# Kernel optimization log

Hardware: AMD Instinct MI355X
Metric: run time of the kernel (lower is better)

The kernel has to match this reference:

```python
import jax, jax.numpy as jnp
import numpy as np

EPS = 1e-8
NUM_HEADS = 8
SCALE = 25.0
SIM_THRESH = 0.75
BLOCK = 10  # per-frame proposal group size used by the zeroing mask


def _l2norm(x):
    return x / (jnp.linalg.norm(x, axis=-1, keepdims=True) + EPS)


def setup_inputs() -> dict:
    key = jax.random.key(0)
    ks = jax.random.split(key, 7)
    B, N, C = 1, 2000, 256
    H = NUM_HEADS
    x_cls = jax.random.normal(ks[0], (B, N, C), dtype=jnp.float32)
    x_reg = jax.random.normal(ks[1], (B, N, C), dtype=jnp.float32)
    cls_score = jax.random.uniform(ks[2], (N,), dtype=jnp.float32)
    fg_score = jax.random.uniform(ks[3], (N,), dtype=jnp.float32)
    coord_attn = jax.random.uniform(ks[4], (B, H, N, N), dtype=jnp.float32)
    W_qkv_cls = jax.random.normal(ks[5], (3 * C, C), dtype=jnp.float32) * 0.02
    W_qkv_reg = jax.random.normal(ks[6], (3 * C, C), dtype=jnp.float32) * 0.02
    return {"x_cls": x_cls, "x_reg": x_reg, "cls_score": cls_score,
            "fg_score": fg_score, "coord_attn": coord_attn,
            "W_qkv_cls": W_qkv_cls, "W_qkv_reg": W_qkv_reg}


def reference(x_cls, x_reg, cls_score, fg_score, coord_attn, W_qkv_cls, W_qkv_reg):
    B, N, C = x_cls.shape
    H = NUM_HEADS
    D = C // H

    def qkv(x, W):
        t = (x @ W.T).reshape(B, N, 3, H, D).transpose(2, 0, 3, 1, 4)  # [3,B,H,N,D]
        return t[0], t[1], t[2]

    q_cls, k_cls, v_cls = qkv(x_cls, W_qkv_cls)
    q_reg, k_reg, v_reg = qkv(x_reg, W_qkv_reg)

    q_cls, k_cls = _l2norm(q_cls), _l2norm(k_cls)
    q_reg, k_reg = _l2norm(q_reg), _l2norm(k_reg)
    v_cls_normed = _l2norm(v_cls)

    cs = cls_score.reshape(1, 1, 1, N)  # broadcast over [B,H,N,N]
    fs = fg_score.reshape(1, 1, 1, N)

    attn_cls_raw = jnp.einsum('bhnd,bhmd->bhnm', v_cls_normed, v_cls_normed)

    attn_cls = jax.nn.softmax(jnp.einsum('bhnd,bhmd->bhnm', q_cls, k_cls) * SCALE * cs, axis=-1)
    attn_reg = jax.nn.softmax(jnp.einsum('bhnd,bhmd->bhnm', q_reg, k_reg) * SCALE * fs, axis=-1)

    attn = (attn_reg + attn_cls) * 0.5 * coord_attn
    attn = jax.lax.stop_gradient(attn)  # original detaches before masking

    # block-diagonal zeroing: row j zeros cols [j//10*10, j//10*10+9), keep diagonal
    rows = jnp.arange(N)[:, None]
    cols = jnp.arange(N)[None, :]
    block_start = (rows // BLOCK) * BLOCK
    zero_mask = (cols >= block_start) & (cols < block_start + (BLOCK - 1)) & (cols != rows)
    attn = jnp.where(zero_mask, 0.0, attn)

    x = jnp.einsum('bhnm,bhmd->bhnd', attn, v_cls).transpose(0, 2, 1, 3).reshape(B, N, C)
    x_ori = v_cls.transpose(0, 2, 1, 3).reshape(B, N, C)
    x_cat = jnp.concatenate([x, x_ori], axis=-1)  # [B,N,2C]

    # ave=True branch
    sim_raw = jnp.sum(attn_cls_raw, axis=1)[0] / H          # [N,N]
    sim_mask = (sim_raw > SIM_THRESH).astype(x_cls.dtype)
    sim_attn = jnp.sum(attn, axis=1)[0] / H                 # [N,N]
    sim_round2 = jax.nn.softmax(sim_attn, axis=-1)
    sim_round2 = sim_mask * sim_round2 / (jnp.sum(sim_mask * sim_round2, axis=-1, keepdims=True) + EPS)
    return x_cat, sim_round2
```

## Files before the change

kernel.cpp:

```cpp
#include <hip/hip_runtime.h>
#include <math.h>

typedef _Float16 half8 __attribute__((ext_vector_type(8)));
typedef _Float16 half4 __attribute__((ext_vector_type(4)));
typedef float f32x4 __attribute__((ext_vector_type(4)));

constexpr int N = 2000;
constexpr int NP = 2048;
constexpr int H = 8;
constexpr int D = 32;
constexpr float SCL = 25.0f;
constexpr float FM = 25.0f;

#define MFMA16(a,b,c) __builtin_amdgcn_mfma_f32_16x16x32_f16((a),(b),(c),0,0,0)


__global__ __launch_bounds__(256) void wconv_kernel(
    const float* __restrict__ Wc, const float* __restrict__ Wr,
    _Float16* __restrict__ Wch, _Float16* __restrict__ Wrh)
{
    const int i = blockIdx.x * 256 + threadIdx.x;
    Wch[i] = (_Float16)Wc[i];
    Wrh[i] = (_Float16)Wr[i];
}

__global__ __launch_bounds__(256) void qkv_kernel(
    const float* __restrict__ xc, const float* __restrict__ xr,
    const _Float16* __restrict__ Wch, const _Float16* __restrict__ Wrh,
    _Float16* __restrict__ Qch, _Float16* __restrict__ Kch,
    _Float16* __restrict__ Qrh, _Float16* __restrict__ Krh,
    _Float16* __restrict__ Vnh, _Float16* __restrict__ Vth,
    float* __restrict__ out)
{
    constexpr int XS = 264;
    __shared__ _Float16 xs[16 * XS];
    const int t = threadIdx.x;
    const int n0 = blockIdx.x * 16;
    const int by = blockIdx.y;
    const int which = (by < 3) ? by : (by - 3);
    const bool isCls = by < 3;
    const float* x = isCls ? xc : xr;
    const _Float16* Wh = isCls ? Wch : Wrh;

    #pragma unroll
    for (int it = 0; it < 4; ++it) {
        const int f = t + it * 256;
        const int row = f >> 6, c4 = f & 63;
        const float4 v = *(const float4*)(x + (size_t)(n0 + row) * 256 + c4 * 4);
        half4 hv; hv[0]=(_Float16)v.x; hv[1]=(_Float16)v.y; hv[2]=(_Float16)v.z; hv[3]=(_Float16)v.w;
        *(half4*)&xs[row * XS + c4 * 4] = hv;
    }
    __syncthreads();

    const int w = t >> 6, l = t & 63;
    const int lr = l & 15, lg = l >> 4;
    const int obase = which * 256 + w * 64;
    f32x4 acc[4] = {{0,0,0,0},{0,0,0,0},{0,0,0,0},{0,0,0,0}};
    for (int k0 = 0; k0 < 256; k0 += 32) {
        const half8 aX = *(const half8*)&xs[lr * XS + k0 + lg * 8];
        #pragma unroll
        for (int s = 0; s < 4; ++s) {
            const half8 bW = *(const half8*)(Wh + (size_t)(obase + s * 16 + lr) * 256 + k0 + lg * 8);
            acc[s] = MFMA16(aX, bW, acc[s]);
        }
    }
    #pragma unroll
    for (int p = 0; p < 2; ++p) {
        const int h = 2 * w + p;
        float ss[4];
        #pragma unroll
        for (int j = 0; j < 4; ++j) {
            float v = acc[2*p][j]*acc[2*p][j] + acc[2*p+1][j]*acc[2*p+1][j];
            #pragma unroll
            for (int off = 1; off < 16; off <<= 1) v += __shfl_xor(v, off);
            ss[j] = sqrtf(v) + 1e-8f;
        }
        if (which < 2) {
            _Float16* Qd = isCls ? (which == 0 ? Qch : Kch) : (which == 0 ? Qrh : Krh);
            #pragma unroll
            for (int sh = 0; sh < 2; ++sh)
                #pragma unroll
                for (int j = 0; j < 4; ++j)
                    Qd[((size_t)h*NP + n0 + lg*4 + j)*D + sh*16 + lr] = (_Float16)(acc[2*p+sh][j] / ss[j]);
        } else {
            #pragma unroll
            for (int sh = 0; sh < 2; ++sh) {
                const int d = sh * 16 + lr;
                half4 tv;
                #pragma unroll
                for (int j = 0; j < 4; ++j) {
                    const float raw = acc[2*p+sh][j];
                    Vnh[((size_t)h*NP + n0 + lg*4 + j)*D + d] = (_Float16)(raw / ss[j]);
                    out[(size_t)(n0 + lg*4 + j)*512 + 256 + h*D + d] = raw;
                    tv[j] = (_Float16)raw;
                }
                *(half4*)(Vth + ((size_t)h*D + d)*NP + n0 + lg*4) = tv;
            }
        }
    }
}

__global__ __launch_bounds__(512) void stats_kernel(
    const _Float16* __restrict__ Qch, const _Float16* __restrict__ Kch,
    const _Float16* __restrict__ Qrh, const _Float16* __restrict__ Krh,
    const float* __restrict__ clsScore, const float* __restrict__ fgScore,
    float* __restrict__ ST)
{
    __shared__ float Ssh[4][2][16];
    const int t = threadIdx.x;
    const int w = t >> 6, l = t & 63;
    const int nsub = w >> 1, mhalf = w & 1;
    const int n0 = blockIdx.x * 64 + nsub * 16;
    const int h = blockIdx.y, z = blockIdx.z;
    const _Float16* Q = z ? Qrh : Qch;
    const _Float16* K = z ? Krh : Kch;
    const float* score = z ? fgScore : clsScore;
    const int lr = l & 15, lg = l >> 4;
    const half8 aQ = *(const half8*)(Q + ((size_t)h*NP + n0 + lr)*D + lg*8);
    float S[4] = {0.f, 0.f, 0.f, 0.f};
    const int msBeg = mhalf ? 63 : 0;
    const int msEnd = mhalf ? 125 : 63;
    for (int ms = msBeg; ms < msEnd; ++ms) {
        const int m = ms * 16 + lr;
        const half8 bK = *(const half8*)(K + ((size_t)h*NP + m)*D + lg*8);
        f32x4 z4 = {0.f, 0.f, 0.f, 0.f};
        const f32x4 c = MFMA16(aQ, bK, z4);
        const float sm = SCL * score[m];
        #pragma unroll
        for (int j = 0; j < 4; ++j) S[j] += __expf(fmaf(c[j], sm, -FM));
    }
    #pragma unroll
    for (int j = 0; j < 4; ++j) {
        #pragma unroll
        for (int off = 1; off < 16; off <<= 1) S[j] += __shfl_xor(S[j], off);
    }
    if (lr == 0) {
        #pragma unroll
        for (int j = 0; j < 4; ++j) Ssh[nsub][mhalf][lg*4 + j] = S[j];
    }
    __syncthreads();
    if (t < 64) {
        const int ns = t >> 4, rl = t & 15;
        ST[((size_t)z*H + h)*NP + blockIdx.x*64 + ns*16 + rl] = Ssh[ns][0][rl] + Ssh[ns][1][rl];
    }
}

__global__ __launch_bounds__(256) void vvmask_kernel(
    const _Float16* __restrict__ Vnh, unsigned char* __restrict__ Mask)
{
    const int t = threadIdx.x;
    const int w = t >> 6, l = t & 63;
    const int n0 = blockIdx.y * 16;
    const int m00 = blockIdx.x * 256 + w * 64;
    const int lr = l & 15, lg = l >> 4;
    half8 aV[8];
    #pragma unroll
    for (int h = 0; h < 8; ++h)
        aV[h] = *(const half8*)(Vnh + ((size_t)(h*NP + n0 + lr))*D + lg*8);
    for (int s = 0; s < 4; ++s) {
        const int mb = m00 + s*16;
        f32x4 acc = {0.f, 0.f, 0.f, 0.f};
        #pragma unroll
        for (int h = 0; h < 8; ++h) {
            const half8 bV = *(const half8*)(Vnh + ((size_t)(h*NP + mb + lr))*D + lg*8);
            acc = MFMA16(aV[h], bV, acc);
        }
        const int m = mb + lr;
        if (m < N) {
            #pragma unroll
            for (int j = 0; j < 4; ++j) {
                const int n = n0 + lg*4 + j;
                Mask[(size_t)n*N + m] = (acc[j]*0.125f > 0.75f) ? (unsigned char)1 : (unsigned char)0;
            }
        }
    }
}

__global__ __launch_bounds__(256) void attn_kernel(
    const _Float16* __restrict__ Qch, const _Float16* __restrict__ Kch,
    const _Float16* __restrict__ Qrh, const _Float16* __restrict__ Krh,
    const _Float16* __restrict__ Vth, const float* __restrict__ coord,
    const float* __restrict__ clsScore, const float* __restrict__ fgScore,
    const float* __restrict__ ST,
    float* __restrict__ SIM, _Float16* __restrict__ XPH)
{
    constexpr int AP = 136;
    __shared__ _Float16 att_s[16 * AP];
    __shared__ _Float16 pvred[4][2][16][18];
    __shared__ float st_s[2][H][16];

    const int t = threadIdx.x;
    const int w = t >> 6, l = t & 63;
    const int mc = blockIdx.x;
    const int m0 = mc * 128;
    const int n0 = blockIdx.y * 16;
    const int lr = l & 15, lg = l >> 4;
    const int colbase = w * 32;

    {
        const int z = t >> 7, h = (t >> 4) & 7, r = t & 15;
        st_s[z][h][r] = 1.f / ST[((size_t)z*H + h)*NP + n0 + r];
    }
    int mI[2]; bool mOk[2]; float sC[2], sF[2];
    #pragma unroll
    for (int s = 0; s < 2; ++s) {
        mI[s] = m0 + colbase + s*16 + lr;
        mOk[s] = mI[s] < N;
        sC[s] = mOk[s] ? SCL * clsScore[mI[s]] : 0.f;
        sF[s] = mOk[s] ? SCL * fgScore[mI[s]] : 0.f;
    }
    int nj[4], bsj[4];
    #pragma unroll
    for (int j = 0; j < 4; ++j) { nj[j] = n0 + lg*4 + j; bsj[j] = (nj[j]/10)*10; }
    float simacc[2][4] = {{0,0,0,0},{0,0,0,0}};
    __syncthreads();

    for (int h = 0; h < H; ++h) {
        float co[2][4];
        #pragma unroll
        for (int s = 0; s < 2; ++s)
            #pragma unroll
            for (int j = 0; j < 4; ++j)
                co[s][j] = mOk[s] ? coord[((size_t)h*N + nj[j])*N + mI[s]] : 0.f;

        const half8 aQc = *(const half8*)(Qch + ((size_t)h*NP + n0 + lr)*D + lg*8);
        const half8 aQr = *(const half8*)(Qrh + ((size_t)h*NP + n0 + lr)*D + lg*8);
        float iC[4], iR[4];
        #pragma unroll
        for (int j = 0; j < 4; ++j) { iC[j] = st_s[0][h][lg*4+j]; iR[j] = st_s[1][h][lg*4+j]; }

        #pragma unroll
        for (int s = 0; s < 2; ++s) {
            const int mb = m0 + colbase + s*16;
            const half8 bKc = *(const half8*)(Kch + ((size_t)h*NP + mb + lr)*D + lg*8);
            const half8 bKr = *(const half8*)(Krh + ((size_t)h*NP + mb + lr)*D + lg*8);
            f32x4 z4 = {0.f, 0.f, 0.f, 0.f};
            const f32x4 cc = MFMA16(aQc, bKc, z4);
            const f32x4 cr = MFMA16(aQr, bKr, z4);
            #pragma unroll
            for (int j = 0; j < 4; ++j) {
                float a = 0.f;
                if (mOk[s]) {
                    const float eC = __expf(fmaf(cc[j], sC[s], -FM)) * iC[j];
                    const float eR = __expf(fmaf(cr[j], sF[s], -FM)) * iR[j];
                    a = (eC + eR) * 0.5f * co[s][j];
                    if (mI[s] >= bsj[j] && mI[s] < bsj[j]+9 && mI[s] != nj[j]) a = 0.f;
                }
                att_s[(lg*4+j)*AP + colbase + s*16 + lr] = (_Float16)a;
                simacc[s][j] += a;
            }
        }
        f32x4 pv0 = {0.f,0.f,0.f,0.f}, pv1 = {0.f,0.f,0.f,0.f};
        {
            const half8 aA  = *(const half8*)&att_s[lr*AP + colbase + lg*8];
            const half8 bV0 = *(const half8*)(Vth + ((size_t)h*D + lr)*NP + m0 + colbase + lg*8);
            const half8 bV1 = *(const half8*)(Vth + ((size_t)h*D + 16 + lr)*NP + m0 + colbase + lg*8);
            pv0 = MFMA16(aA, bV0, pv0);
            pv1 = MFMA16(aA, bV1, pv1);
        }
        #pragma unroll
        for (int j = 0; j < 4; ++j) {
            pvred[w][0][lg*4+j][lr] = (_Float16)pv0[j];
            pvred[w][1][lg*4+j][lr] = (_Float16)pv1[j];
        }
        __syncthreads();
        #pragma unroll
        for (int e = t; e < 512; e += 256) {
            const int db = e >> 8, r = (e >> 4) & 15, d0 = e & 15;
            const float sum = (float)pvred[0][db][r][d0] + (float)pvred[1][db][r][d0]
                            + (float)pvred[2][db][r][d0] + (float)pvred[3][db][r][d0];
            XPH[(((size_t)mc*H + h)*N + n0 + r)*D + db*16 + d0] = (_Float16)sum;
        }
        __syncthreads();
    }
    #pragma unroll
    for (int s = 0; s < 2; ++s) {
        if (!mOk[s]) continue;
        #pragma unroll
        for (int j = 0; j < 4; ++j)
            SIM[(size_t)nj[j]*N + mI[s]] = simacc[s][j] * 0.125f;
    }
}

__global__ __launch_bounds__(256) void reduce_kernel(
    const _Float16* __restrict__ XPH, float* __restrict__ out)
{
    const int n = blockIdx.x, t = threadIdx.x;
    const int h = t >> 5, d = t & 31;
    float acc = 0.f;
    #pragma unroll
    for (int mcI = 0; mcI < 16; ++mcI)
        acc += (float)XPH[(((size_t)mcI*H + h)*N + n)*D + d];
    out[(size_t)n*512 + t] = acc;
}

__global__ __launch_bounds__(256) void simfinal_kernel(
    const float* __restrict__ SIM, const unsigned char* __restrict__ Mask,
    float* __restrict__ out)
{
    __shared__ float4 buf[500];
    __shared__ float redA[4], redB[4];
    const int n = blockIdx.x, t = threadIdx.x;
    const float4* row4 = (const float4*)(SIM + (size_t)n*N);
    const uchar4* mrow4 = (const uchar4*)(Mask + (size_t)n*N);
    float mx = -1e30f;
    for (int i = t; i < 500; i += 256) {
        const float4 v = row4[i];
        buf[i] = v;
        mx = fmaxf(mx, fmaxf(fmaxf(v.x, v.y), fmaxf(v.z, v.w)));
    }
    #pragma unroll
    for (int off = 1; off < 64; off <<= 1) mx = fmaxf(mx, __shfl_xor(mx, off));
    const int wv = t >> 6;
    if ((t & 63) == 0) redA[wv] = mx;
    __syncthreads();
    const float M = fmaxf(fmaxf(redA[0], redA[1]), fmaxf(redA[2], redA[3]));
    float sA = 0.f, sM = 0.f;
    for (int i = t; i < 500; i += 256) {
        float4 v = buf[i];
        const uchar4 mk = mrow4[i];
        v.x = __expf(v.x - M); v.y = __expf(v.y - M);
        v.z = __expf(v.z - M); v.w = __expf(v.w - M);
        buf[i] = v;
        sA += v.x + v.y + v.z + v.w;
        sM += (mk.x ? v.x : 0.f) + (mk.y ? v.y : 0.f) + (mk.z ? v.z : 0.f) + (mk.w ? v.w : 0.f);
    }
    #pragma unroll
    for (int off = 1; off < 64; off <<= 1) { sA += __shfl_xor(sA, off); sM += __shfl_xor(sM, off); }
    __syncthreads();
    if ((t & 63) == 0) { redA[wv] = sA; redB[wv] = sM; }
    __syncthreads();
    const float SA = redA[0] + redA[1] + redA[2] + redA[3];
    const float SMK = redB[0] + redB[1] + redB[2] + redB[3];
    const float inv = 1.f / (SMK + 1e-8f * SA);
    float4* orow = (float4*)(out + 1024000 + (size_t)n*N);
    for (int i = t; i < 500; i += 256) {
        const float4 v = buf[i];
        const uchar4 mk = mrow4[i];
        orow[i] = make_float4(mk.x ? v.x * inv : 0.f, mk.y ? v.y * inv : 0.f,
                              mk.z ? v.z * inv : 0.f, mk.w ? v.w * inv : 0.f);
    }
}

extern "C" void kernel_launch(void* const* d_in, const int* in_sizes, int n_in,
                              void* d_out, int out_size, void* d_ws, size_t ws_size,
                              hipStream_t stream) {
    const float* x_cls     = (const float*)d_in[0];
    const float* x_reg     = (const float*)d_in[1];
    const float* cls_score = (const float*)d_in[2];
    const float* fg_score  = (const float*)d_in[3];
    const float* coord     = (const float*)d_in[4];
    const float* Wc        = (const float*)d_in[5];
    const float* Wr        = (const float*)d_in[6];

    char* base = (char*)d_ws;
    float* ST       = (float*)base;
    float* SIM      = (float*)(base + 131072);
    _Float16* XPH   = (_Float16*)(base + 16131072);
    _Float16* Qch   = (_Float16*)(base + 32515072);
    _Float16* Kch   = Qch + 524288;
    _Float16* Qrh   = Qch + 2*524288;
    _Float16* Krh   = Qch + 3*524288;
    _Float16* Vnh   = Qch + 4*524288;
    _Float16* Vth   = Qch + 5*524288;
    _Float16* Wch   = (_Float16*)(base + 38806528);
    _Float16* Wrh   = (_Float16*)(base + 39199744);
    unsigned char* Mask = (unsigned char*)(base + 39592960);
    float* out = (float*)d_out;

    hipMemsetAsync(Qch, 0, 6*1048576, stream);
    wconv_kernel<<<768, 256, 0, stream>>>(Wc, Wr, Wch, Wrh);
    qkv_kernel<<<dim3(125, 5), 256, 0, stream>>>(x_cls, x_reg, Wch, Wrh,
                                                 Qch, Kch, Qrh, Krh, Vnh, Vth, out);
    stats_kernel<<<dim3(32, 8, 2), 512, 0, stream>>>(Qch, Kch, Qrh, Krh, cls_score, fg_score, ST);
    vvmask_kernel<<<dim3(8, 125), 256, 0, stream>>>(Vnh, Mask);
    attn_kernel<<<dim3(16, 125), 256, 0, stream>>>(Qch, Kch, Qrh, Krh, Vth, coord,
                                                   cls_score, fg_score, ST, SIM, XPH);
    reduce_kernel<<<2000, 256, 0, stream>>>(XPH, out);
    simfinal_kernel<<<2000, 256, 0, stream>>>(SIM, Mask, out);
}
```

Measured before the change: 137.6 us.

## Transpose attention MFMA layout to keep scores in registers and remove LDS round-trip

The QK MFMA operands are swapped so each lane holds four consecutive key columns for one query row. The attention fragment then feeds the PV MFMA (16x16x16) directly from registers, with no LDS staging of att_s. This also allows vectorized coalesced coord, score and SIM accesses, plus prefetching of the next head's coord tile. Per-head barriers are dropped by keeping all head partials in a larger LDS buffer and reducing once at the end. Each block now covers 256 columns, halving the XPH partials, and the stats kernel stores reciprocals. The trade-offs are more registers and more LDS per block.

```diff
diff --git a/kernel.cpp b/kernel.cpp
--- a/kernel.cpp
+++ b/kernel.cpp
@@ -12,7 +12,8 @@
 constexpr float SCL = 25.0f;
 constexpr float FM = 25.0f;
 
-#define MFMA16(a,b,c) __builtin_amdgcn_mfma_f32_16x16x32_f16((a),(b),(c),0,0,0)
+#define MFMA16(a,b,c)  __builtin_amdgcn_mfma_f32_16x16x32_f16((a),(b),(c),0,0,0)
+#define MFMA16K(a,b,c) __builtin_amdgcn_mfma_f32_16x16x16f16((a),(b),(c),0,0,0)
 
 
 __global__ __launch_bounds__(256) void wconv_kernel(
@@ -104,7 +105,7 @@
     const _Float16* __restrict__ Qch, const _Float16* __restrict__ Kch,
     const _Float16* __restrict__ Qrh, const _Float16* __restrict__ Krh,
     const float* __restrict__ clsScore, const float* __restrict__ fgScore,
-    float* __restrict__ ST)
+    float* __restrict__ STi)
 {
     __shared__ float Ssh[4][2][16];
     const int t = threadIdx.x;
@@ -141,7 +142,8 @@
     __syncthreads();
     if (t < 64) {
         const int ns = t >> 4, rl = t & 15;
-        ST[((size_t)z*H + h)*NP + blockIdx.x*64 + ns*16 + rl] = Ssh[ns][0][rl] + Ssh[ns][1][rl];
+        STi[((size_t)z*H + h)*NP + blockIdx.x*64 + ns*16 + rl]
+            = 1.f / (Ssh[ns][0][rl] + Ssh[ns][1][rl]);
     }
 }
 
@@ -181,104 +183,101 @@
     const _Float16* __restrict__ Qrh, const _Float16* __restrict__ Krh,
     const _Float16* __restrict__ Vth, const float* __restrict__ coord,
     const float* __restrict__ clsScore, const float* __restrict__ fgScore,
-    const float* __restrict__ ST,
+    const float* __restrict__ STi,
     float* __restrict__ SIM, _Float16* __restrict__ XPH)
 {
-    constexpr int AP = 136;
-    __shared__ _Float16 att_s[16 * AP];
-    __shared__ _Float16 pvred[4][2][16][18];
-    __shared__ float st_s[2][H][16];
+    __shared__ _Float16 pvred[4][H][2][16][17];
 
     const int t = threadIdx.x;
     const int w = t >> 6, l = t & 63;
+    const int lr = l & 15, lg = l >> 4;
     const int mc = blockIdx.x;
-    const int m0 = mc * 128;
+    const int m0 = mc * 256;
     const int n0 = blockIdx.y * 16;
-    const int lr = l & 15, lg = l >> 4;
-    const int colbase = w * 32;
-
-    {
-        const int z = t >> 7, h = (t >> 4) & 7, r = t & 15;
-        st_s[z][h][r] = 1.f / ST[((size_t)z*H + h)*NP + n0 + r];
-    }
-    int mI[2]; bool mOk[2]; float sC[2], sF[2];
-    #pragma unroll
-    for (int s = 0; s < 2; ++s) {
-        mI[s] = m0 + colbase + s*16 + lr;
-        mOk[s] = mI[s] < N;
-        sC[s] = mOk[s] ? SCL * clsScore[mI[s]] : 0.f;
-        sF[s] = mOk[s] ? SCL * fgScore[mI[s]] : 0.f;
-    }
-    int nj[4], bsj[4];
-    #pragma unroll
-    for (int j = 0; j < 4; ++j) { nj[j] = n0 + lg*4 + j; bsj[j] = (nj[j]/10)*10; }
-    float simacc[2][4] = {{0,0,0,0},{0,0,0,0}};
-    __syncthreads();
+    const int n  = n0 + lr;
+    const int bs = (n / 10) * 10;
+    const int cb = w * 64;
+
+    int mb[4]; bool ok[4];
+    #pragma unroll
+    for (int s = 0; s < 4; ++s) { mb[s] = m0 + cb + s*16; ok[s] = mb[s] < N; }
+
+    float simacc[4][4];
+    #pragma unroll
+    for (int s = 0; s < 4; ++s)
+        #pragma unroll
+        for (int j = 0; j < 4; ++j) simacc[s][j] = 0.f;
+
+    f32x4 co[4];
+    #pragma unroll
+    for (int s = 0; s < 4; ++s)
+        co[s] = ok[s] ? *(const f32x4*)(coord + (size_t)n*N + mb[s] + lg*4)
+                      : (f32x4){0.f,0.f,0.f,0.f};
 
     for (int h = 0; h < H; ++h) {
-        float co[2][4];
-        #pragma unroll
-        for (int s = 0; s < 2; ++s)
-            #pragma unroll
-            for (int j = 0; j < 4; ++j)
-                co[s][j] = mOk[s] ? coord[((size_t)h*N + nj[j])*N + mI[s]] : 0.f;
-
-        const half8 aQc = *(const half8*)(Qch + ((size_t)h*NP + n0 + lr)*D + lg*8);
-        const half8 aQr = *(const half8*)(Qrh + ((size_t)h*NP + n0 + lr)*D + lg*8);
-        float iC[4], iR[4];
-        #pragma unroll
-        for (int j = 0; j < 4; ++j) { iC[j] = st_s[0][h][lg*4+j]; iR[j] = st_s[1][h][lg*4+j]; }
-
-        #pragma unroll
-        for (int s = 0; s < 2; ++s) {
-            const int mb = m0 + colbase + s*16;
-            const half8 bKc = *(const half8*)(Kch + ((size_t)h*NP + mb + lr)*D + lg*8);
-            const half8 bKr = *(const half8*)(Krh + ((size_t)h*NP + mb + lr)*D + lg*8);
-            f32x4 z4 = {0.f, 0.f, 0.f, 0.f};
-            const f32x4 cc = MFMA16(aQc, bKc, z4);
-            const f32x4 cr = MFMA16(aQr, bKr, z4);
+        f32x4 coN[4];
+        if (h < H-1) {
+            #pragma unroll
+            for (int s = 0; s < 4; ++s)
+                coN[s] = ok[s] ? *(const f32x4*)(coord + ((size_t)(h+1)*N + n)*N + mb[s] + lg*4)
+                               : (f32x4){0.f,0.f,0.f,0.f};
+        }
+        const float iC = STi[((size_t)0*H + h)*NP + n];
+        const float iR = STi[((size_t)1*H + h)*NP + n];
+        const half8 aQc = *(const half8*)(Qch + ((size_t)h*NP + n)*D + lg*8);
+        const half8 aQr = *(const half8*)(Qrh + ((size_t)h*NP + n)*D + lg*8);
+
+        f32x4 pv0 = {0.f,0.f,0.f,0.f}, pv1 = {0.f,0.f,0.f,0.f};
+        #pragma unroll
+        for (int s = 0; s < 4; ++s) {
+            if (!ok[s]) continue;
+            const half8 bKc = *(const half8*)(Kch + ((size_t)h*NP + mb[s] + lr)*D + lg*8);
+            const half8 bKr = *(const half8*)(Krh + ((size_t)h*NP + mb[s] + lr)*D + lg*8);
+            f32x4 z4 = {0.f,0.f,0.f,0.f};
+            const f32x4 cc = MFMA16(bKc, aQc, z4);
+            const f32x4 cr = MFMA16(bKr, aQr, z4);
+            const f32x4 sc4 = *(const f32x4*)(clsScore + mb[s] + lg*4);
+            const f32x4 sf4 = *(const f32x4*)(fgScore + mb[s] + lg*4);
+            half4 af;
             #pragma unroll
             for (int j = 0; j < 4; ++j) {
-                float a = 0.f;
-                if (mOk[s]) {
-                    const float eC = __expf(fmaf(cc[j], sC[s], -FM)) * iC[j];
-                    const float eR = __expf(fmaf(cr[j], sF[s], -FM)) * iR[j];
-                    a = (eC + eR) * 0.5f * co[s][j];
-                    if (mI[s] >= bsj[j] && mI[s] < bsj[j]+9 && mI[s] != nj[j]) a = 0.f;
-                }
-                att_s[(lg*4+j)*AP + colbase + s*16 + lr] = (_Float16)a;
+                const int m = mb[s] + lg*4 + j;
+                float a = (__expf(fmaf(cc[j], SCL*sc4[j], -FM)) * iC
+                         + __expf(fmaf(cr[j], SCL*sf4[j], -FM)) * iR) * 0.5f * co[s][j];
+                if (m >= bs && m < bs+9 && m != n) a = 0.f;
                 simacc[s][j] += a;
+                af[j] = (_Float16)a;
             }
-        }
-        f32x4 pv0 = {0.f,0.f,0.f,0.f}, pv1 = {0.f,0.f,0.f,0.f};
-        {
-            const half8 aA  = *(const half8*)&att_s[lr*AP + colbase + lg*8];
-            const half8 bV0 = *(const half8*)(Vth + ((size_t)h*D + lr)*NP + m0 + colbase + lg*8);
-            const half8 bV1 = *(const half8*)(Vth + ((size_t)h*D + 16 + lr)*NP + m0 + colbase + lg*8);
-            pv0 = MFMA16(aA, bV0, pv0);
-            pv1 = MFMA16(aA, bV1, pv1);
+            const half4 bV0 = *(const half4*)(Vth + ((size_t)h*D + lr)*NP + mb[s] + lg*4);
+            const half4 bV1 = *(const half4*)(Vth + ((size_t)h*D + 16 + lr)*NP + mb[s] + lg*4);
+            pv0 = MFMA16K(af, bV0, pv0);
+            pv1 = MFMA16K(af, bV1, pv1);
         }
         #pragma unroll
         for (int j = 0; j < 4; ++j) {
-            pvred[w][0][lg*4+j][lr] = (_Float16)pv0[j];
-            pvred[w][1][lg*4+j][lr] = (_Float16)pv1[j];
-        }
-        __syncthreads();
-        #pragma unroll
-        for (int e = t; e < 512; e += 256) {
-            const int db = e >> 8, r = (e >> 4) & 15, d0 = e & 15;
-            const float sum = (float)pvred[0][db][r][d0] + (float)pvred[1][db][r][d0]
-                            + (float)pvred[2][db][r][d0] + (float)pvred[3][db][r][d0];
-            XPH[(((size_t)mc*H + h)*N + n0 + r)*D + db*16 + d0] = (_Float16)sum;
-        }
-        __syncthreads();
-    }
-    #pragma unroll
-    for (int s = 0; s < 2; ++s) {
-        if (!mOk[s]) continue;
-        #pragma unroll
-        for (int j = 0; j < 4; ++j)
-            SIM[(size_t)nj[j]*N + mI[s]] = simacc[s][j] * 0.125f;
+            pvred[w][h][0][lg*4 + j][lr] = (_Float16)pv0[j];
+            pvred[w][h][1][lg*4 + j][lr] = (_Float16)pv1[j];
+        }
+        #pragma unroll
+        for (int s = 0; s < 4; ++s) co[s] = coN[s];
+    }
+
+    __syncthreads();
+
+    for (int e = t; e < 4096; e += 256) {
+        const int hh = e >> 9, db = (e >> 8) & 1, r = (e >> 4) & 15, d0 = e & 15;
+        const float sum = (float)pvred[0][hh][db][r][d0] + (float)pvred[1][hh][db][r][d0]
+                        + (float)pvred[2][hh][db][r][d0] + (float)pvred[3][hh][db][r][d0];
+        XPH[(((size_t)mc*H + hh)*N + n0 + r)*D + db*16 + d0] = (_Float16)sum;
+    }
+
+    #pragma unroll
+    for (int s = 0; s < 4; ++s) {
+        if (!ok[s]) continue;
+        f32x4 v;
+        #pragma unroll
+        for (int j = 0; j < 4; ++j) v[j] = simacc[s][j] * 0.125f;
+        *(f32x4*)(SIM + (size_t)n*N + mb[s] + lg*4) = v;
     }
 }
 
@@ -289,7 +288,7 @@
     const int h = t >> 5, d = t & 31;
     float acc = 0.f;
     #pragma unroll
-    for (int mcI = 0; mcI < 16; ++mcI)
+    for (int mcI = 0; mcI < 8; ++mcI)
         acc += (float)XPH[(((size_t)mcI*H + h)*N + n)*D + d];
     out[(size_t)n*512 + t] = acc;
 }
@@ -354,28 +353,28 @@
     const float* Wr        = (const float*)d_in[6];
 
     char* base = (char*)d_ws;
-    float* ST       = (float*)base;
+    float* STi      = (float*)base;
     float* SIM      = (float*)(base + 131072);
     _Float16* XPH   = (_Float16*)(base + 16131072);
-    _Float16* Qch   = (_Float16*)(base + 32515072);
+    _Float16* Qch   = (_Float16*)(base + 24323072);
     _Float16* Kch   = Qch + 524288;
     _Float16* Qrh   = Qch + 2*524288;
     _Float16* Krh   = Qch + 3*524288;
     _Float16* Vnh   = Qch + 4*524288;
     _Float16* Vth   = Qch + 5*524288;
-    _Float16* Wch   = (_Float16*)(base + 38806528);
-    _Float16* Wrh   = (_Float16*)(base + 39199744);
-    unsigned char* Mask = (unsigned char*)(base + 39592960);
+    _Float16* Wch   = (_Float16*)(base + 30614528);
+    _Float16* Wrh   = (_Float16*)(base + 31007744);
+    unsigned char* Mask = (unsigned char*)(base + 31400960);
     float* out = (float*)d_out;
 
     hipMemsetAsync(Qch, 0, 6*1048576, stream);
     wconv_kernel<<<768, 256, 0, stream>>>(Wc, Wr, Wch, Wrh);
     qkv_kernel<<<dim3(125, 5), 256, 0, stream>>>(x_cls, x_reg, Wch, Wrh,
                                                  Qch, Kch, Qrh, Krh, Vnh, Vth, out);
-    stats_kernel<<<dim3(32, 8, 2), 512, 0, stream>>>(Qch, Kch, Qrh, Krh, cls_score, fg_score, ST);
+    stats_kernel<<<dim3(32, 8, 2), 512, 0, stream>>>(Qch, Kch, Qrh, Krh, cls_score, fg_score, STi);
     vvmask_kernel<<<dim3(8, 125), 256, 0, stream>>>(Vnh, Mask);
-    attn_kernel<<<dim3(16, 125), 256, 0, stream>>>(Qch, Kch, Qrh, Krh, Vth, coord,
-                                                   cls_score, fg_score, ST, SIM, XPH);
+    attn_kernel<<<dim3(8, 125), 256, 0, stream>>>(Qch, Kch, Qrh, Krh, Vth, coord,
+                                                  cls_score, fg_score, STi, SIM, XPH);
     reduce_kernel<<<2000, 256, 0, stream>>>(XPH, out);
     simfinal_kernel<<<2000, 256, 0, stream>>>(SIM, Mask, out);
 }
```

Result: slower. 165.3 us (+20.2%).
